# Kernel optimization log

Hardware: AMD Instinct MI355X
Metric: run time of the kernel (lower is better)

## Reference

```python
import jax, jax.numpy as jnp
import numpy as np

B, S, D = 8, 1024, 768
H = 12
DH = D // H  # 64
SCALE = 1.0 / (D ** 0.5)  # module scales by full embedding_dim, not head_dim


def setup_inputs() -> dict:
    key = jax.random.key(0)
    ks = jax.random.split(key, 7)
    std = 1.0 / np.sqrt(D)
    return {
        "x": jax.random.normal(ks[0], (B, S, D), dtype=jnp.float32),
        "Wq": jax.random.uniform(ks[1], (D, D), jnp.float32, -std, std),
        "bq": jax.random.uniform(ks[2], (D,), jnp.float32, -std, std),
        "Wk": jax.random.uniform(ks[3], (D, D), jnp.float32, -std, std),
        "bk": jax.random.uniform(ks[4], (D,), jnp.float32, -std, std),
        "Wv": jax.random.uniform(ks[5], (D, D), jnp.float32, -std, std),
        "bv": jax.random.uniform(ks[6], (D,), jnp.float32, -std, std),
    }


def reference(x, Wq, bq, Wk, bk, Wv, bv):
    b, s, d = x.shape
    # projections; torch.chunk(dim=-1) == reshape last dim to [H, DH]
    q = (x @ Wq + bq).reshape(b, s, H, DH)
    k = (x @ Wk + bk).reshape(b, s, H, DH)
    v = (x @ Wv + bv).reshape(b, s, H, DH)
    # per-head scores [b, h, s, s], scaled by sqrt(embedding_dim) per source
    scores = jnp.einsum("bqhd,bkhd->bhqk", q, k) * SCALE
    attn = jax.nn.softmax(scores, axis=-1)
    out = jnp.einsum("bhqk,bkhd->bqhd", attn, v)
    # concat heads back along last dim (order matches chunk order)
    return out.reshape(b, s, d)
```

## Files before the change

### kernel.cpp

```cpp
#include <hip/hip_runtime.h>
#include <cstdint>
#include <cstddef>

typedef unsigned short u16;
typedef unsigned int u32;
typedef unsigned char u8;

using bfx8 = __attribute__((ext_vector_type(8))) __bf16;
using floatx16 = __attribute__((ext_vector_type(16))) float;

static constexpr int kS = 1024;
static constexpr int kD = 768;
static constexpr int kH = 12;
static constexpr int kDH = 64;
#define SCALE 0.036084391824351614f

__device__ __forceinline__ u16 f2bf(float f) {
    u32 u = __float_as_uint(f);
    return (u16)((u + 0x7fffu + ((u >> 16) & 1u)) >> 16);
}

__device__ __forceinline__ void gld16(const void* g, void* l) {
    __builtin_amdgcn_global_load_lds(
        (__attribute__((address_space(1))) const u32*)g,
        (__attribute__((address_space(3))) u32*)l, 16, 0, 0);
}

__global__ __launch_bounds__(256) void cvt(const float* __restrict__ x, u16* __restrict__ xb,
                                           const float* __restrict__ w0, const float* __restrict__ w1,
                                           const float* __restrict__ w2, u16* __restrict__ wt) {
    __shared__ float t[32][33];
    int bid = blockIdx.x;
    if (bid < 6144) {
        int i = (bid * 256 + threadIdx.x) * 4;
        float4 v = *(const float4*)(x + i);
        u32 lo = (u32)f2bf(v.x) | ((u32)f2bf(v.y) << 16);
        u32 hi = (u32)f2bf(v.z) | ((u32)f2bf(v.w) << 16);
        *(uint2*)(xb + i) = make_uint2(lo, hi);
    } else {
        int idx = bid - 6144;
        int z = idx / 576;
        int rem = idx - z * 576;
        int by = rem / 24, bx = rem - by * 24;
        const float* W = z == 0 ? w0 : (z == 1 ? w1 : w2);
        u16* dst = wt + (size_t)z * kD * kD;
        int k0 = bx * 32, n0 = by * 32;
        int tx = threadIdx.x & 31, ty = threadIdx.x >> 5;
#pragma unroll
        for (int j = 0; j < 4; j++)
            t[ty + j * 8][tx] = W[(size_t)(k0 + ty + j * 8) * kD + n0 + tx];
        __syncthreads();
#pragma unroll
        for (int j = 0; j < 4; j++)
            dst[(size_t)(n0 + ty + j * 8) * kD + k0 + tx] = f2bf(t[tx][ty + j * 8]);
    }
}

__global__ __launch_bounds__(256) void proj(const u16* __restrict__ xb, const u16* __restrict__ wt,
                                            const float* __restrict__ bq, const float* __restrict__ bk,
                                            const float* __restrict__ bvp,
                                            u16* __restrict__ qb, u16* __restrict__ kb, u16* __restrict__ vt) {
    __shared__ u16 As0[128 * 64];
    __shared__ u16 Bs0[128 * 64];
    __shared__ u16 As1[128 * 64];
    __shared__ u16 Bs1[128 * 64];
    int orig = blockIdx.x;
    int wg = (orig & 7) * 144 + (orig >> 3);
    int mt = wg / 18, nt = wg - mt * 18;
    int m0 = mt * 128;
    int n0g = nt * 128;
    int t = threadIdx.x;
    int w = t >> 6, lane = t & 63;
    int l31 = lane & 31, hi = lane >> 5;
    int wm = (w & 1) * 64, wn = (w >> 1) * 64;
    int rloc8 = lane >> 3, p8 = lane & 7;
    int chw = p8 ^ rloc8;
    const u16* Brow = wt + (size_t)n0g * kD;
    int swz = l31 & 7;
    floatx16 acc[2][2] = {};

    auto STAGE = [&](u16* Ad, u16* Bd, int ks) {
#pragma unroll
        for (int i = 0; i < 4; i++) {
            int j = w * 4 + i;
            int r = 8 * j + rloc8;
            gld16(xb + (size_t)(m0 + r) * kD + ks + chw * 8, Ad + j * 512);
            gld16(Brow + (size_t)r * kD + ks + chw * 8, Bd + j * 512);
        }
    };
    auto COMP = [&](const u16* Ad, const u16* Bd) {
#pragma unroll
        for (int s = 0; s < 4; s++) {
            int tc = ((s * 2 + hi) ^ swz) * 8;
            bfx8 a[2], bf[2];
#pragma unroll
            for (int i = 0; i < 2; i++) {
                a[i] = *(const bfx8*)&Ad[(wm + i * 32 + l31) * 64 + tc];
                bf[i] = *(const bfx8*)&Bd[(wn + i * 32 + l31) * 64 + tc];
            }
#pragma unroll
            for (int i = 0; i < 2; i++)
#pragma unroll
                for (int j2 = 0; j2 < 2; j2++)
                    acc[i][j2] = __builtin_amdgcn_mfma_f32_32x32x16_bf16(a[i], bf[j2], acc[i][j2], 0, 0, 0);
        }
    };

    STAGE(As0, Bs0, 0);
    __syncthreads();
    for (int kk = 0; kk < 5; kk++) {
        STAGE(As1, Bs1, 64 + 128 * kk);
        COMP(As0, Bs0);
        __syncthreads();
        STAGE(As0, Bs0, 128 + 128 * kk);
        COMP(As1, Bs1);
        __syncthreads();
    }
    STAGE(As1, Bs1, 704);
    COMP(As0, Bs0);
    __syncthreads();
    COMP(As1, Bs1);

    int zz = nt / 6;
    int nl0 = (nt - zz * 6) * 128;
    const float* bias = zz == 0 ? bq : (zz == 1 ? bk : bvp);
    float mul = zz == 0 ? SCALE : 1.0f;
#pragma unroll
    for (int j = 0; j < 2; j++) {
        int nl = nl0 + wn + j * 32 + l31;
        float bb = bias[nl];
#pragma unroll
        for (int i = 0; i < 2; i++) {
            int mbase = m0 + wm + i * 32 + 4 * hi;
            if (zz < 2) {
                u16* dst = zz == 0 ? qb : kb;
#pragma unroll
                for (int reg = 0; reg < 16; reg++) {
                    int m = mbase + (reg & 3) + 8 * (reg >> 2);
                    dst[(size_t)m * kD + nl] = f2bf((acc[i][j][reg] + bb) * mul);
                }
            } else {
                int hh = nl >> 6, dh = nl & 63;
#pragma unroll
                for (int g = 0; g < 4; g++) {
                    int m = (m0 + wm + i * 32) + 4 * (g & 1) + 8 * hi + 16 * (g >> 1);
                    int bi = m >> 10, s = m & 1023;
                    u32 lo = (u32)f2bf(acc[i][j][4 * g + 0] + bb) | ((u32)f2bf(acc[i][j][4 * g + 1] + bb) << 16);
                    u32 h2 = (u32)f2bf(acc[i][j][4 * g + 2] + bb) | ((u32)f2bf(acc[i][j][4 * g + 3] + bb) << 16);
                    *(uint2*)&vt[(((size_t)bi * kH + hh) * kDH + dh) * kS + s] = make_uint2(lo, h2);
                }
            }
        }
    }
}

__global__ __launch_bounds__(256, 3) void attn(const u16* __restrict__ qb, const u16* __restrict__ kb,
                                               const u16* __restrict__ vt, float* __restrict__ out) {
    __shared__ u16 Ks[128 * 64];
    __shared__ u16 Vs[64 * 128];
    __shared__ float Lw[128];
    int orig = blockIdx.x;
    int wg = (orig & 7) * 96 + (orig >> 3);
    int bh = wg >> 3;
    int q0 = (wg & 7) * 128;
    int b = bh / kH, h = bh % kH;
    int t = threadIdx.x, w = t >> 6, lane = t & 63;
    int l31 = lane & 31, hi = lane >> 5;
    int swz = l31 & 7;

    bfx8 qf[4];
    {
        const u16* qrow = qb + (size_t)(b * kS + q0 + w * 32 + l31) * kD + h * kDH + hi * 8;
#pragma unroll
        for (int f = 0; f < 4; f++) qf[f] = *(const bfx8*)(qrow + f * 16);
    }

    float rsum = 0.f;
    floatx16 oacc[2] = {};

    for (int kt = 0; kt < 8; kt++) {
        int kk0 = kt * 128;
        __syncthreads();
#pragma unroll
        for (int i = 0; i < 4; i++) {
            int jj = 4 * w + i;
            int r = 8 * jj + (lane >> 3);
            int c = (lane & 7) ^ ((lane >> 3) & 7);
            gld16(kb + (size_t)(b * kS + kk0 + r) * kD + h * kDH + c * 8, &Ks[jj * 512]);
        }
#pragma unroll
        for (int i = 0; i < 4; i++) {
            int jj = 4 * w + i;
            int r = 4 * jj + (lane >> 4);
            int c = (lane & 15) ^ (r & 15);
            gld16(vt + (((size_t)b * kH + h) * kDH + r) * kS + kk0 + c * 8, &Vs[jj * 512]);
        }
        __syncthreads();

        floatx16 sacc[4] = {};
#pragma unroll
        for (int s2 = 0; s2 < 4; s2++) {
#pragma unroll
            for (int fm = 0; fm < 4; fm++) {
                bfx8 ak = *(const bfx8*)&Ks[(fm * 32 + l31) * 64 + ((s2 * 2 + hi) ^ swz) * 8];
                sacc[fm] = __builtin_amdgcn_mfma_f32_32x32x16_bf16(ak, qf[s2], sacc[fm], 0, 0, 0);
            }
        }

        bfx8 pa[4][2];
#pragma unroll
        for (int fm = 0; fm < 4; fm++) {
#pragma unroll
            for (int hh = 0; hh < 2; hh++) {
                bfx8 pv;
#pragma unroll
                for (int jj = 0; jj < 8; jj++) {
                    float e = __expf(sacc[fm][8 * hh + jj]);
                    rsum += e;
                    pv[jj] = (__bf16)e;
                }
                pa[fm][hh] = pv;
            }
        }

#pragma unroll
        for (int s = 0; s < 8; s++) {
#pragma unroll
            for (int db = 0; db < 2; db++) {
                bfx8 bv = *(const bfx8*)((const u8*)Vs + (db * 32 + l31) * 256 + (((s * 2 + hi) ^ (l31 & 15)) * 16));
                oacc[db] = __builtin_amdgcn_mfma_f32_32x32x16_bf16(pa[s >> 1][s & 1], bv, oacc[db], 0, 0, 0);
            }
        }
    }

    rsum += __shfl_xor(rsum, 32, 64);
    if (lane < 32) Lw[w * 32 + lane] = rsum;
    __syncthreads();
#pragma unroll
    for (int g = 0; g < 4; g++) {
#pragma unroll
        for (int r2 = 0; r2 < 4; r2++) {
            int qloc = w * 32 + 4 * hi + r2 + 8 * g;
            float linv = 1.0f / Lw[qloc];
#pragma unroll
            for (int db = 0; db < 2; db++) {
                out[(size_t)(b * kS + q0 + qloc) * kD + h * kDH + db * 32 + l31] = oacc[db][4 * g + r2] * linv;
            }
        }
    }
}

extern "C" void kernel_launch(void* const* d_in, const int* in_sizes, int n_in,
                              void* d_out, int out_size, void* d_ws, size_t ws_size,
                              hipStream_t stream) {
    const float* x  = (const float*)d_in[0];
    const float* Wq = (const float*)d_in[1];
    const float* bq = (const float*)d_in[2];
    const float* Wk = (const float*)d_in[3];
    const float* bk = (const float*)d_in[4];
    const float* Wv = (const float*)d_in[5];
    const float* bv = (const float*)d_in[6];
    float* out = (float*)d_out;

    u16* ws = (u16*)d_ws;
    u16* xb = ws;
    u16* wt = xb + 6291456;
    u16* qb = wt + 1769472;
    u16* kb = qb + 6291456;
    u16* vt = kb + 6291456;

    cvt<<<dim3(7872), dim3(256), 0, stream>>>(x, xb, Wq, Wk, Wv, wt);
    proj<<<dim3(1152), dim3(256), 0, stream>>>(xb, wt, bq, bk, bv, qb, kb, vt);
    attn<<<dim3(768), dim3(256), 0, stream>>>(qb, kb, vt, out);
}
```

Measured before the change: 165.8 us.

## Enlarge projection GEMM tiles to 256x256 with phased load/MFMA interleaving and setprio

Rewrites the QKV projection GEMM to use 256x256 tiles with 512-thread blocks. Each K step is split into four phases, and each phase issues part of the next tile's global-to-LDS loads. Partial vmcnt waits and raw s_barriers replace full syncthreads. MFMA sections run under s_setprio in both proj and attention, so wave priority favours matrix work. The aim is more data reuse per tile and finer load/compute overlap, at the cost of far fewer blocks (288 instead of 1152), which risks a tail effect and uneven CU load.

```diff
diff --git a/kernel.cpp b/kernel.cpp
--- a/kernel.cpp
+++ b/kernel.cpp
@@ -25,6 +25,9 @@
         (__attribute__((address_space(1))) const u32*)g,
         (__attribute__((address_space(3))) u32*)l, 16, 0, 0);
 }
+
+#define VMW(n) asm volatile("s_waitcnt vmcnt(" #n ")" ::: "memory")
+#define LGKM0 asm volatile("s_waitcnt lgkmcnt(0)" ::: "memory")
 
 __global__ __launch_bounds__(256) void cvt(const float* __restrict__ x, u16* __restrict__ xb,
                                            const float* __restrict__ w0, const float* __restrict__ w1,
@@ -56,102 +59,122 @@
     }
 }
 
-__global__ __launch_bounds__(256) void proj(const u16* __restrict__ xb, const u16* __restrict__ wt,
-                                            const float* __restrict__ bq, const float* __restrict__ bk,
-                                            const float* __restrict__ bvp,
-                                            u16* __restrict__ qb, u16* __restrict__ kb, u16* __restrict__ vt) {
-    __shared__ u16 As0[128 * 64];
-    __shared__ u16 Bs0[128 * 64];
-    __shared__ u16 As1[128 * 64];
-    __shared__ u16 Bs1[128 * 64];
+__global__ __launch_bounds__(512, 2) void proj(const u16* __restrict__ xb, const u16* __restrict__ wt,
+                                               const float* __restrict__ bq, const float* __restrict__ bk,
+                                               const float* __restrict__ bvp,
+                                               u16* __restrict__ qb, u16* __restrict__ kb, u16* __restrict__ vt) {
+    __shared__ u16 As0[256 * 64];
+    __shared__ u16 Bs0[256 * 64];
+    __shared__ u16 As1[256 * 64];
+    __shared__ u16 Bs1[256 * 64];
     int orig = blockIdx.x;
-    int wg = (orig & 7) * 144 + (orig >> 3);
-    int mt = wg / 18, nt = wg - mt * 18;
-    int m0 = mt * 128;
-    int n0g = nt * 128;
+    int wg = (orig & 7) * 36 + (orig >> 3);
+    int mt = wg / 9, nt = wg - mt * 9;
+    int m0 = mt * 256;
     int t = threadIdx.x;
     int w = t >> 6, lane = t & 63;
     int l31 = lane & 31, hi = lane >> 5;
-    int wm = (w & 1) * 64, wn = (w >> 1) * 64;
-    int rloc8 = lane >> 3, p8 = lane & 7;
-    int chw = p8 ^ rloc8;
-    const u16* Brow = wt + (size_t)n0g * kD;
+    int wm = (w & 1) * 128, wn = (w >> 1) * 64;
+    int rowt = t >> 3;
+    int ch8 = ((t & 7) ^ (rowt & 7)) * 8;
+    const u16* Arow = xb + (size_t)m0 * kD;
+    const u16* Brow = wt + (size_t)(nt * 256) * kD;
     int swz = l31 & 7;
-    floatx16 acc[2][2] = {};
-
-    auto STAGE = [&](u16* Ad, u16* Bd, int ks) {
-#pragma unroll
-        for (int i = 0; i < 4; i++) {
-            int j = w * 4 + i;
-            int r = 8 * j + rloc8;
-            gld16(xb + (size_t)(m0 + r) * kD + ks + chw * 8, Ad + j * 512);
-            gld16(Brow + (size_t)r * kD + ks + chw * 8, Bd + j * 512);
-        }
-    };
-    auto COMP = [&](const u16* Ad, const u16* Bd) {
-#pragma unroll
-        for (int s = 0; s < 4; s++) {
-            int tc = ((s * 2 + hi) ^ swz) * 8;
-            bfx8 a[2], bf[2];
-#pragma unroll
-            for (int i = 0; i < 2; i++) {
-                a[i] = *(const bfx8*)&Ad[(wm + i * 32 + l31) * 64 + tc];
-                bf[i] = *(const bfx8*)&Bd[(wn + i * 32 + l31) * 64 + tc];
-            }
-#pragma unroll
-            for (int i = 0; i < 2; i++)
-#pragma unroll
-                for (int j2 = 0; j2 < 2; j2++)
-                    acc[i][j2] = __builtin_amdgcn_mfma_f32_32x32x16_bf16(a[i], bf[j2], acc[i][j2], 0, 0, 0);
-        }
-    };
-
-    STAGE(As0, Bs0, 0);
-    __syncthreads();
-    for (int kk = 0; kk < 5; kk++) {
-        STAGE(As1, Bs1, 64 + 128 * kk);
-        COMP(As0, Bs0);
-        __syncthreads();
-        STAGE(As0, Bs0, 128 + 128 * kk);
-        COMP(As1, Bs1);
-        __syncthreads();
-    }
-    STAGE(As1, Bs1, 704);
-    COMP(As0, Bs0);
-    __syncthreads();
-    COMP(As1, Bs1);
-
-    int zz = nt / 6;
-    int nl0 = (nt - zz * 6) * 128;
+    int tc[4];
+#pragma unroll
+    for (int s_ = 0; s_ < 4; s_++) tc[s_] = ((s_ * 2 + hi) ^ swz) * 8;
+    floatx16 acc[4][2] = {};
+    bfx8 bfr[2][4];
+
+#define STG(DB, SRC, U, KSN) \
+    gld16((SRC) + (size_t)(64 * (U) + rowt) * kD + (KSN) + ch8, (DB) + (U) * 4096 + w * 512)
+
+#define PHASE(RA, RB, MI, STAGES, VMN)                                          \
+    {                                                                           \
+        bfx8 af[4];                                                             \
+        const u16* ar_ = (RA) + (wm + (MI) * 32 + l31) * 64;                    \
+        _Pragma("unroll")                                                       \
+        for (int s_ = 0; s_ < 4; s_++) af[s_] = *(const bfx8*)(ar_ + tc[s_]);   \
+        if ((MI) == 0) {                                                        \
+            _Pragma("unroll")                                                   \
+            for (int ni_ = 0; ni_ < 2; ni_++) {                                 \
+                const u16* br_ = (RB) + (wn + ni_ * 32 + l31) * 64;             \
+                _Pragma("unroll")                                               \
+                for (int s_ = 0; s_ < 4; s_++)                                  \
+                    bfr[ni_][s_] = *(const bfx8*)(br_ + tc[s_]);                \
+            }                                                                   \
+        }                                                                       \
+        STAGES;                                                                 \
+        __builtin_amdgcn_sched_barrier(0);                                      \
+        VMN;                                                                    \
+        __builtin_amdgcn_s_barrier();                                           \
+        LGKM0;                                                                  \
+        __builtin_amdgcn_s_setprio(1);                                          \
+        _Pragma("unroll")                                                       \
+        for (int s_ = 0; s_ < 4; s_++)                                          \
+            _Pragma("unroll")                                                   \
+            for (int ni_ = 0; ni_ < 2; ni_++)                                   \
+                acc[MI][ni_] = __builtin_amdgcn_mfma_f32_32x32x16_bf16(         \
+                    af[s_], bfr[ni_][s_], acc[MI][ni_], 0, 0, 0);               \
+        __builtin_amdgcn_s_setprio(0);                                          \
+        __builtin_amdgcn_s_barrier();                                           \
+    }
+
+#define ITERK(RA, RB, WA, WB, KSN)                                                        \
+    PHASE(RA, RB, 0, { STG(WA, Arow, 0, KSN); STG(WA, Arow, 2, KSN); }, )                 \
+    PHASE(RA, RB, 1, { STG(WB, Brow, 0, KSN); STG(WB, Brow, 1, KSN); }, VMW(4))           \
+    PHASE(RA, RB, 2, { STG(WB, Brow, 2, KSN); STG(WB, Brow, 3, KSN); }, )                 \
+    PHASE(RA, RB, 3, { STG(WA, Arow, 1, KSN); STG(WA, Arow, 3, KSN); }, VMW(2))
+
+#pragma unroll
+    for (int u = 0; u < 4; u++) {
+        STG(As0, Arow, u, 0);
+        STG(Bs0, Brow, u, 0);
+    }
+    VMW(0);
+    __builtin_amdgcn_s_barrier();
+
+    for (int kp = 0; kp < 6; kp++) {
+        int kn1 = kp * 128 + 64;
+        int kn2 = kp * 128 + 128;
+        ITERK(As0, Bs0, As1, Bs1, kn1)
+        ITERK(As1, Bs1, As0, Bs0, kn2)
+    }
+
+    int zz = nt / 3;
+    int nl0 = (nt - zz * 3) * 256;
     const float* bias = zz == 0 ? bq : (zz == 1 ? bk : bvp);
     float mul = zz == 0 ? SCALE : 1.0f;
 #pragma unroll
-    for (int j = 0; j < 2; j++) {
-        int nl = nl0 + wn + j * 32 + l31;
+    for (int ni = 0; ni < 2; ni++) {
+        int nl = nl0 + wn + ni * 32 + l31;
         float bb = bias[nl];
 #pragma unroll
-        for (int i = 0; i < 2; i++) {
-            int mbase = m0 + wm + i * 32 + 4 * hi;
+        for (int mi = 0; mi < 4; mi++) {
             if (zz < 2) {
+                int mbase = m0 + wm + mi * 32 + 4 * hi;
                 u16* dst = zz == 0 ? qb : kb;
 #pragma unroll
                 for (int reg = 0; reg < 16; reg++) {
                     int m = mbase + (reg & 3) + 8 * (reg >> 2);
-                    dst[(size_t)m * kD + nl] = f2bf((acc[i][j][reg] + bb) * mul);
+                    dst[(size_t)m * kD + nl] = f2bf((acc[mi][ni][reg] + bb) * mul);
                 }
             } else {
                 int hh = nl >> 6, dh = nl & 63;
 #pragma unroll
                 for (int g = 0; g < 4; g++) {
-                    int m = (m0 + wm + i * 32) + 4 * (g & 1) + 8 * hi + 16 * (g >> 1);
+                    int m = (m0 + wm + mi * 32) + 4 * (g & 1) + 8 * hi + 16 * (g >> 1);
                     int bi = m >> 10, s = m & 1023;
-                    u32 lo = (u32)f2bf(acc[i][j][4 * g + 0] + bb) | ((u32)f2bf(acc[i][j][4 * g + 1] + bb) << 16);
-                    u32 h2 = (u32)f2bf(acc[i][j][4 * g + 2] + bb) | ((u32)f2bf(acc[i][j][4 * g + 3] + bb) << 16);
+                    u32 lo = (u32)f2bf(acc[mi][ni][4 * g + 0] + bb) | ((u32)f2bf(acc[mi][ni][4 * g + 1] + bb) << 16);
+                    u32 h2 = (u32)f2bf(acc[mi][ni][4 * g + 2] + bb) | ((u32)f2bf(acc[mi][ni][4 * g + 3] + bb) << 16);
                     *(uint2*)&vt[(((size_t)bi * kH + hh) * kDH + dh) * kS + s] = make_uint2(lo, h2);
                 }
             }
         }
     }
+#undef STG
+#undef PHASE
+#undef ITERK
 }
 
 __global__ __launch_bounds__(256, 3) void attn(const u16* __restrict__ qb, const u16* __restrict__ kb,
@@ -198,6 +221,7 @@
         __syncthreads();
 
         floatx16 sacc[4] = {};
+        __builtin_amdgcn_s_setprio(1);
 #pragma unroll
         for (int s2 = 0; s2 < 4; s2++) {
 #pragma unroll
@@ -206,6 +230,7 @@
                 sacc[fm] = __builtin_amdgcn_mfma_f32_32x32x16_bf16(ak, qf[s2], sacc[fm], 0, 0, 0);
             }
         }
+        __builtin_amdgcn_s_setprio(0);
 
         bfx8 pa[4][2];
 #pragma unroll
@@ -223,6 +248,7 @@
             }
         }
 
+        __builtin_amdgcn_s_setprio(1);
 #pragma unroll
         for (int s = 0; s < 8; s++) {
 #pragma unroll
@@ -231,6 +257,7 @@
                 oacc[db] = __builtin_amdgcn_mfma_f32_32x32x16_bf16(pa[s >> 1][s & 1], bv, oacc[db], 0, 0, 0);
             }
         }
+        __builtin_amdgcn_s_setprio(0);
     }
 
     rsum += __shfl_xor(rsum, 32, 64);
@@ -270,6 +297,6 @@
     u16* vt = kb + 6291456;
 
     cvt<<<dim3(7872), dim3(256), 0, stream>>>(x, xb, Wq, Wk, Wv, wt);
-    proj<<<dim3(1152), dim3(256), 0, stream>>>(xb, wt, bq, bk, bv, qb, kb, vt);
+    proj<<<dim3(288), dim3(512), 0, stream>>>(xb, wt, bq, bk, bv, qb, kb, vt);
     attn<<<dim3(768), dim3(256), 0, stream>>>(qb, kb, vt, out);
 }
```

New measurement: 178.9 us. 1.08x slower.
